# Kernel optimization log

Hardware: AMD Instinct MI355X
Metric: run time of the kernel (lower is better)

The kernel has to match this reference:

```python
import jax, jax.numpy as jnp
import numpy as np

N, D, H, L, E, P = 50000, 128, 128, 3, 640000, 100000


def setup_inputs() -> dict:
    key = jax.random.key(0)
    ks = jax.random.split(key, 10)
    x = jax.random.normal(ks[0], (N, D), dtype=jnp.float32)
    ei = jax.random.randint(ks[1], (2, E), 0, N, dtype=jnp.int64)
    pos = jax.random.randint(ks[2], (2, P), 0, N, dtype=jnp.int64)
    neg = jax.random.randint(ks[3], (2, P), 0, N, dtype=jnp.int64)
    # GCN weights: layer0 is [D,H], rest [H,H]; D==H so stack as [L,H,H]
    gcn_w = jax.random.normal(ks[4], (L, H, H), dtype=jnp.float32) / np.sqrt(H)
    gcn_b = jnp.zeros((L, H), dtype=jnp.float32)
    pred_w = jax.random.normal(ks[5], (H * L, 1), dtype=jnp.float32) / np.sqrt(H * L)
    pred_b = jnp.zeros((1,), dtype=jnp.float32)
    return {"x": x, "ei": ei, "pos": pos, "neg": neg,
            "gcn_w": gcn_w, "gcn_b": gcn_b, "pred_w": pred_w, "pred_b": pred_b}


def reference(x, ei, pos, neg, gcn_w, gcn_b, pred_w, pred_b):
    n = x.shape[0]
    loops = jnp.arange(n, dtype=ei.dtype)
    src = jnp.concatenate([ei[0], loops])  # self-loops (GCNConv default)
    dst = jnp.concatenate([ei[1], loops])
    deg = jax.ops.segment_sum(jnp.ones_like(dst, dtype=x.dtype), dst, num_segments=n)
    dinv = jax.lax.rsqrt(deg)  # deg >= 1 thanks to self-loops
    coef = (dinv[src] * dinv[dst])[:, None]  # [E+N, 1] symmetric norm

    embs = []
    h = x
    for i in range(gcn_w.shape[0]):
        hw = h @ gcn_w[i]                                   # [N, H]
        agg = jax.ops.segment_sum(hw[src] * coef, dst, num_segments=n)
        h = jax.nn.relu(agg + gcn_b[i])
        embs.append(h)
    z = jnp.concatenate(embs, axis=1)                        # [N, H*L]

    def logits(e):
        return (z[e[0]] * z[e[1]]) @ pred_w + pred_b         # [P, 1]

    pos_logit = logits(pos)
    neg_logit = logits(neg)
    # BCEWithLogitsLoss with targets [1...1, 0...0], mean reduction
    total = pos_logit.shape[0] + neg_logit.shape[0]
    loss = (jnp.sum(-jax.nn.log_sigmoid(pos_logit)) +
            jnp.sum(-jax.nn.log_sigmoid(-neg_logit))) / total
    return loss
```

## Files before the change

### kernel.cpp

```cpp
#include <hip/hip_runtime.h>
#include <hip/hip_bf16.h>

#define DD 128

typedef __attribute__((ext_vector_type(8))) short short8;
typedef __attribute__((ext_vector_type(4))) float f32x4;
typedef __attribute__((ext_vector_type(2))) float f32x2;

static __device__ __forceinline__ int gtid() {
    return blockIdx.x * blockDim.x + threadIdx.x;
}

static __device__ __forceinline__ ushort f2bfu(float f) {
    __hip_bfloat16 h = __float2bfloat16(f);
    return *reinterpret_cast<ushort*>(&h);
}

static __device__ __forceinline__ unsigned int fp8e(float f) {
    unsigned int s = (__float_as_uint(f) >> 31) << 7;
    float a = fabsf(f);
    if (a < 0.015625f) return s | (unsigned int)rintf(a * 512.0f);
    unsigned int u = __float_as_uint(a);
    u += 0x0007FFFFu + ((u >> 20) & 1u);
    unsigned int e8 = (u >> 23) - 120u;
    unsigned int m = (u >> 20) & 7u;
    if (e8 > 15u || (e8 == 15u && m == 7u)) return s | 0x7Eu;
    return s | (e8 << 3) | m;
}

static __device__ __forceinline__ float fp8d(unsigned int b) {
    unsigned int t = b & 0x7Fu;
    float v = (t >= 8u) ? __uint_as_float((t << 20) + 0x3C000000u)
                        : (float)t * 0.001953125f;
    return (b & 0x80u) ? -v : v;
}

static __device__ __forceinline__ unsigned int pk8x2(float a, float b) {
#if __has_builtin(__builtin_amdgcn_cvt_pk_fp8_f32)
    return (unsigned int)__builtin_amdgcn_cvt_pk_fp8_f32(a, b, 0, false);
#else
    return fp8e(a) | (fp8e(b) << 8);
#endif
}

static __device__ __forceinline__ unsigned int pk8x4(float a, float b, float c, float d) {
#if __has_builtin(__builtin_amdgcn_cvt_pk_fp8_f32)
    int v = __builtin_amdgcn_cvt_pk_fp8_f32(a, b, 0, false);
    v = __builtin_amdgcn_cvt_pk_fp8_f32(c, d, v, true);
    return (unsigned int)v;
#else
    return fp8e(a) | (fp8e(b) << 8) | (fp8e(c) << 16) | (fp8e(d) << 24);
#endif
}

static __device__ __forceinline__ void fp8x4_dec(unsigned int u, float* f) {
#if __has_builtin(__builtin_amdgcn_cvt_pk_f32_fp8)
    f32x2 lo = __builtin_amdgcn_cvt_pk_f32_fp8((int)u, false);
    f32x2 hi = __builtin_amdgcn_cvt_pk_f32_fp8((int)u, true);
    f[0] = lo[0]; f[1] = lo[1]; f[2] = hi[0]; f[3] = hi[1];
#else
    f[0] = fp8d(u & 0xFFu);
    f[1] = fp8d((u >> 8) & 0xFFu);
    f[2] = fp8d((u >> 16) & 0xFFu);
    f[3] = fp8d((u >> 24) & 0xFFu);
#endif
}


__global__ void count_kernel(int* __restrict__ counts, const int* __restrict__ dst, int e) {
    int i = gtid();
    if (i < e) atomicAdd(&counts[dst[i]], 1);
}

__global__ __launch_bounds__(256) void scan_blocks(const int* __restrict__ counts,
                                                   int* __restrict__ rowptr,
                                                   int* __restrict__ partial,
                                                   float* __restrict__ dinv, int n) {
    __shared__ int s[256];
    int i = blockIdx.x * 256 + threadIdx.x;
    int v = (i < n) ? counts[i] : 0;
    if (i < n) dinv[i] = rsqrtf(1.0f + (float)v);
    s[threadIdx.x] = v;
    __syncthreads();
    for (int off = 1; off < 256; off <<= 1) {
        int t = (threadIdx.x >= off) ? s[threadIdx.x - off] : 0;
        __syncthreads();
        s[threadIdx.x] += t;
        __syncthreads();
    }
    if (i < n) rowptr[i] = s[threadIdx.x] - v;
    if (threadIdx.x == 255) partial[blockIdx.x] = s[255];
}

__global__ __launch_bounds__(256) void scan_partials(int* __restrict__ partial,
                                                     int* __restrict__ partial2, int nb) {
    __shared__ int s[256];
    int v = (threadIdx.x < nb) ? partial[threadIdx.x] : 0;
    s[threadIdx.x] = v;
    __syncthreads();
    for (int off = 1; off < 256; off <<= 1) {
        int t = (threadIdx.x >= off) ? s[threadIdx.x - off] : 0;
        __syncthreads();
        s[threadIdx.x] += t;
        __syncthreads();
    }
    partial2[threadIdx.x] = s[threadIdx.x] - v;
}

__global__ __launch_bounds__(256) void add_offsets(int* __restrict__ rowptr,
                                                   int* __restrict__ cursor,
                                                   const int* __restrict__ partial2,
                                                   int n, int e) {
    int i = blockIdx.x * 256 + threadIdx.x;
    if (i < n) {
        int r = rowptr[i] + partial2[blockIdx.x];
        rowptr[i] = r;
        cursor[i] = r;
        if (i == n - 1) rowptr[n] = e;
    }
}

__global__ __launch_bounds__(256) void fill_kernel(
    const int* __restrict__ ei, int* __restrict__ cursor,
    ushort* __restrict__ csr_src, int e, int n, int blocksPerPart) {
    int part = blockIdx.x & 7;
    int blk = blockIdx.x >> 3;
    int lo = (int)(((long)n * part) >> 3);
    int hi = (int)(((long)n * (part + 1)) >> 3);
    int stride = blocksPerPart * 256;
    for (int i = blk * 256 + threadIdx.x; i < e; i += stride) {
        int d = ei[e + i];
        if (d < lo || d >= hi) continue;
        int s = ei[i];
        int pos = atomicAdd(&cursor[d], 1);
        csr_src[pos] = (ushort)s;
    }
}

__global__ void cvt_kernel(const float* __restrict__ x, unsigned char* __restrict__ xq, size_t m8) {
    size_t i = (size_t)blockIdx.x * blockDim.x + threadIdx.x;
    if (i >= m8) return;
    const float4* xp = reinterpret_cast<const float4*>(x + i * 8);
    float4 a = xp[0], b = xp[1];
    uint2 q;
    q.x = pk8x4(a.x, a.y, a.z, a.w);
    q.y = pk8x4(b.x, b.y, b.z, b.w);
    *reinterpret_cast<uint2*>(xq + i * 8) = q;
}

__global__ __launch_bounds__(256) void wpack_kernel(const float* __restrict__ gcn_w,
                                                    ushort* __restrict__ wfrag) {
    int tid = blockIdx.x * 256 + threadIdx.x;
    if (tid >= 3 * 4 * 8 * 64) return;
    int lane = tid & 63;
    int c = (tid >> 6) & 7;
    int s = (tid >> 9) & 3;
    int l = tid >> 11;
    const float* W = gcn_w + (size_t)l * 128 * 128;
    int col = c * 16 + (lane & 15);
    int k0 = s * 32 + (lane >> 4) * 8;
    ushort u[8];
#pragma unroll
    for (int j = 0; j < 8; ++j) {
        u[j] = f2bfu(W[(size_t)(k0 + j) * 128 + col]);
    }
    *reinterpret_cast<uint4*>(wfrag + (size_t)tid * 8) = *reinterpret_cast<const uint4*>(u);
}

__global__ __launch_bounds__(256) void layer_fused_kernel(
    const unsigned char* __restrict__ srcq, int srcStride,
    const int* __restrict__ rowptr, const ushort* __restrict__ csr_src,
    const float* __restrict__ dinv, const ushort* __restrict__ wfrag,
    const float* __restrict__ bias, const float* __restrict__ pwsl,
    unsigned char* __restrict__ zq_sl, unsigned char* __restrict__ zqw_sl, int n) {
    __shared__ unsigned char ah[16 * 256];
    int lane = threadIdx.x & 63;
    int wid = threadIdx.x >> 6;
    int row0 = blockIdx.x * 16;

    short8 b0[4], b1[4];
    int c0 = wid * 2;
#pragma unroll
    for (int s = 0; s < 4; ++s) {
        b0[s] = *reinterpret_cast<const short8*>(wfrag + ((size_t)(s * 8 + c0) * 64 + lane) * 8);
        b1[s] = *reinterpret_cast<const short8*>(wfrag + ((size_t)(s * 8 + c0 + 1) * 64 + lane) * 8);
    }

    int g = lane >> 3;
    int c = lane & 7;
#pragma unroll
    for (int t = 0; t < 4; ++t) {
        int lr = wid * 4 + t;
        int row = row0 + lr;
        int j0 = rowptr[row], j1 = rowptr[row + 1];
        float dr = dinv[row];
        float acc[16];
#pragma unroll
        for (int k = 0; k < 16; ++k) acc[k] = 0.f;
        for (int j = j0 + g; j < j1; j += 8) {
            int s = (int)csr_src[j];
            float cf = dinv[s] * dr;
            uint4 v = *reinterpret_cast<const uint4*>(srcq + (size_t)s * srcStride + c * 16);
            float f[16];
            fp8x4_dec(v.x, f);
            fp8x4_dec(v.y, f + 4);
            fp8x4_dec(v.z, f + 8);
            fp8x4_dec(v.w, f + 12);
#pragma unroll
            for (int k = 0; k < 16; ++k) acc[k] = fmaf(cf, f[k], acc[k]);
        }
#pragma unroll
        for (int k = 0; k < 16; ++k) {
            acc[k] += __shfl_xor(acc[k], 8);
            acc[k] += __shfl_xor(acc[k], 16);
            acc[k] += __shfl_xor(acc[k], 32);
        }
        float d2 = dr * dr;
        uint4 sv = *reinterpret_cast<const uint4*>(srcq + (size_t)row * srcStride + c * 16);
        float sf[16];
        fp8x4_dec(sv.x, sf);
        fp8x4_dec(sv.y, sf + 4);
        fp8x4_dec(sv.z, sf + 8);
        fp8x4_dec(sv.w, sf + 12);
#pragma unroll
        for (int k = 0; k < 16; ++k) acc[k] = fmaf(d2, sf[k], acc[k]);
        if (g == 0) {
            unsigned int pk[8];
#pragma unroll
            for (int q = 0; q < 8; ++q) {
                pk[q] = (unsigned int)f2bfu(acc[2 * q]) | ((unsigned int)f2bfu(acc[2 * q + 1]) << 16);
            }
            int swz = (lr & 7) << 4;
            int bo = c * 32;
            *reinterpret_cast<uint4*>(ah + lr * 256 + (bo ^ swz)) =
                *reinterpret_cast<const uint4*>(pk);
            *reinterpret_cast<uint4*>(ah + lr * 256 + ((bo + 16) ^ swz)) =
                *reinterpret_cast<const uint4*>(pk + 4);
        }
    }
    __syncthreads();

    int rlo = lane & 15;
    int kg = lane >> 4;
    int swzr = (rlo & 7) << 4;
    const unsigned char* arow = ah + rlo * 256;
    short8 a0 = *reinterpret_cast<const short8*>(arow + ((kg * 16) ^ swzr));
    short8 a1 = *reinterpret_cast<const short8*>(arow + ((kg * 16 + 64) ^ swzr));
    short8 a2 = *reinterpret_cast<const short8*>(arow + ((kg * 16 + 128) ^ swzr));
    short8 a3 = *reinterpret_cast<const short8*>(arow + ((kg * 16 + 192) ^ swzr));
    f32x4 acc0 = {0.f, 0.f, 0.f, 0.f};
    f32x4 acc1 = {0.f, 0.f, 0.f, 0.f};
    acc0 = __builtin_amdgcn_mfma_f32_16x16x32_bf16(a0, b0[0], acc0, 0, 0, 0);
    acc1 = __builtin_amdgcn_mfma_f32_16x16x32_bf16(a0, b1[0], acc1, 0, 0, 0);
    acc0 = __builtin_amdgcn_mfma_f32_16x16x32_bf16(a1, b0[1], acc0, 0, 0, 0);
    acc1 = __builtin_amdgcn_mfma_f32_16x16x32_bf16(a1, b1[1], acc1, 0, 0, 0);
    acc0 = __builtin_amdgcn_mfma_f32_16x16x32_bf16(a2, b0[2], acc0, 0, 0, 0);
    acc1 = __builtin_amdgcn_mfma_f32_16x16x32_bf16(a2, b1[2], acc1, 0, 0, 0);
    acc0 = __builtin_amdgcn_mfma_f32_16x16x32_bf16(a3, b0[3], acc0, 0, 0, 0);
    acc1 = __builtin_amdgcn_mfma_f32_16x16x32_bf16(a3, b1[3], acc1, 0, 0, 0);

    int col0 = wid * 32 + rlo;
    float bias0 = bias[col0], bias1 = bias[col0 + 16];
    float pw0 = pwsl[col0] * 8.0f, pw1 = pwsl[col0 + 16] * 8.0f;
    int rowBase = row0 + kg * 4;
#pragma unroll
    for (int r = 0; r < 4; ++r) {
        float v0 = fmaxf(acc0[r] + bias0, 0.f);
        float v1 = fmaxf(acc1[r] + bias1, 0.f);
        unsigned int q = pk8x2(v0, v1);
        unsigned char* zr = zq_sl + (size_t)(rowBase + r) * 384 + col0;
        zr[0] = (unsigned char)(q & 0xFFu);
        zr[16] = (unsigned char)((q >> 8) & 0xFFu);
        unsigned int w = pk8x2(v0 * pw0, v1 * pw1);
        unsigned char* wr = zqw_sl + (size_t)(rowBase + r) * 384 + col0;
        wr[0] = (unsigned char)(w & 0xFFu);
        wr[16] = (unsigned char)((w >> 8) & 0xFFu);
    }
}

__global__ __launch_bounds__(256) void loss_mfma_kernel(
    const unsigned char* __restrict__ zq, const unsigned char* __restrict__ zqw,
    const int* __restrict__ pos, const int* __restrict__ neg,
    const float* __restrict__ pb, float* __restrict__ partialOut,
    int p, float inv_total) {
    __shared__ float red[4];
    int lane = threadIdx.x & 63;
    int wv = threadIdx.x >> 6;
    int pairBase = (blockIdx.x * 4 + wv) * 16;
    float term = 0.f;
    if (pairBase < 2 * p) {
        int m = lane & 15;
        int kg = lane >> 4;
        int pi = pairBase + m;
        int pic = (pi < 2 * p) ? pi : (2 * p - 1);
        bool isneg = (pic >= p);
        const int* pr = isneg ? neg : pos;
        int idx = isneg ? (pic - p) : pic;
        int a = pr[idx];
        int b = pr[p + idx];
        const long* pa = reinterpret_cast<const long*>(zq + (size_t)a * 384) + kg;
        const long* pbw = reinterpret_cast<const long*>(zqw + (size_t)b * 384) + kg;
        long av[12], bv[12];
#pragma unroll
        for (int s = 0; s < 12; ++s) av[s] = pa[s * 4];
#pragma unroll
        for (int s = 0; s < 12; ++s) bv[s] = pbw[s * 4];
        f32x4 acc = {0.f, 0.f, 0.f, 0.f};
#pragma unroll
        for (int s = 0; s < 12; ++s) {
            acc = __builtin_amdgcn_mfma_f32_16x16x32_fp8_fp8(av[s], bv[s], acc, 0, 0, 0);
        }
        bool isdiag = (lane >> 4) == ((lane & 15) >> 2);
        int r2 = lane & 3;
        float v = (r2 == 0) ? acc[0] : (r2 == 1) ? acc[1] : (r2 == 2) ? acc[2] : acc[3];
        if (isdiag && pi < 2 * p) {
            float logit = v * 0.125f + pb[0];
            float t = isneg ? logit : -logit;
            term = (fmaxf(t, 0.f) + log1pf(expf(-fabsf(t)))) * inv_total;
        }
    }
#pragma unroll
    for (int off = 1; off < 64; off <<= 1) term += __shfl_xor(term, off);
    if (lane == 0) red[wv] = term;
    __syncthreads();
    if (threadIdx.x == 0) partialOut[blockIdx.x] = red[0] + red[1] + red[2] + red[3];
}

__global__ __launch_bounds__(256) void loss_reduce_kernel(
    const float* __restrict__ partial, float* __restrict__ out, int m) {
    __shared__ float s[256];
    float a = 0.f;
    for (int i = threadIdx.x; i < m; i += 256) a += partial[i];
    s[threadIdx.x] = a;
    __syncthreads();
    for (int off = 128; off > 0; off >>= 1) {
        if (threadIdx.x < off) s[threadIdx.x] += s[threadIdx.x + off];
        __syncthreads();
    }
    if (threadIdx.x == 0) out[0] = s[0];
}

extern "C" void kernel_launch(void* const* d_in, const int* in_sizes, int n_in,
                              void* d_out, int out_size, void* d_ws, size_t ws_size,
                              hipStream_t stream) {
    const float* x      = (const float*)d_in[0];
    const int*   ei     = (const int*)d_in[1];
    const int*   pos    = (const int*)d_in[2];
    const int*   neg    = (const int*)d_in[3];
    const float* gcn_w  = (const float*)d_in[4];
    const float* gcn_b  = (const float*)d_in[5];
    const float* pred_w = (const float*)d_in[6];
    const float* pred_b = (const float*)d_in[7];
    float* out = (float*)d_out;

    const int n = in_sizes[0] / DD;
    const int e = in_sizes[1] / 2;
    const int p = in_sizes[2] / 2;
    const int nb = (n + 255) / 256;

    char* ws = (char*)d_ws;
    size_t off = 0;
    auto alloc = [&](size_t bytes) {
        void* ptr = ws + off;
        off += (bytes + 255) & ~(size_t)255;
        return ptr;
    };
    float* dinv      = (float*)alloc((size_t)n * 4);
    int*   counts    = (int*)alloc((size_t)n * 4);
    int*   rowptr    = (int*)alloc((size_t)(n + 1) * 4);
    int*   cursor    = (int*)alloc((size_t)n * 4);
    int*   partial   = (int*)alloc(256 * 4);
    int*   partial2  = (int*)alloc(256 * 4);
    float* lossPart  = (float*)alloc((size_t)4096 * 4);
    ushort* csr_src  = (ushort*)alloc((size_t)e * 2);
    ushort* wfrag    = (ushort*)alloc((size_t)3 * 2048 * 8 * 2);
    unsigned char* xq = (unsigned char*)alloc((size_t)n * 128);
    unsigned char* zq  = (unsigned char*)alloc((size_t)n * 384);
    unsigned char* zqw = (unsigned char*)alloc((size_t)n * 384);
    (void)ws_size;

    hipMemsetAsync(counts, 0, (size_t)n * 4, stream);

    count_kernel<<<(e + 255) / 256, 256, 0, stream>>>(counts, ei + e, e);
    scan_blocks<<<nb, 256, 0, stream>>>(counts, rowptr, partial, dinv, n);
    scan_partials<<<1, 256, 0, stream>>>(partial, partial2, nb);
    add_offsets<<<nb, 256, 0, stream>>>(rowptr, cursor, partial2, n, e);
    int blocksPerPart = (e + 255) / 256 / 2;
    fill_kernel<<<blocksPerPart * 8, 256, 0, stream>>>(ei, cursor, csr_src, e, n, blocksPerPart);

    size_t m8 = (size_t)n * 128 / 8;
    cvt_kernel<<<(int)((m8 + 255) / 256), 256, 0, stream>>>(x, xq, m8);
    wpack_kernel<<<24, 256, 0, stream>>>(gcn_w, wfrag);

    const int layerBlocks = n / 16;
    for (int l = 0; l < 3; ++l) {
        const unsigned char* srcq = (l == 0) ? xq : (zq + (size_t)(l - 1) * 128);
        int srcStride = (l == 0) ? 128 : 384;
        layer_fused_kernel<<<layerBlocks, 256, 0, stream>>>(
            srcq, srcStride, rowptr, csr_src, dinv,
            wfrag + (size_t)l * 2048 * 8,
            gcn_b + (size_t)l * 128, pred_w + (size_t)l * 128,
            zq + (size_t)l * 128, zqw + (size_t)l * 128, n);
    }

    float inv_total = 1.0f / (2.0f * (float)p);
    int lossBlocks = (2 * p + 63) / 64;
    loss_mfma_kernel<<<lossBlocks, 256, 0, stream>>>(
        zq, zqw, pos, neg, pred_b, lossPart, p, inv_total);
    loss_reduce_kernel<<<1, 256, 0, stream>>>(lossPart, out, lossBlocks);
}
```

Measured before the change: 264.0 us.

## Use 1024-thread blocks with one wave per row in fused GCN layer

The fused layer kernel moves from 256 threads (4 waves, each aggregating 4 rows serially) to 1024 threads (16 waves, each aggregating one row). After the barrier, 8 waves each compute one 16-column MFMA tile and the other 8 exit. This exposes more parallel gather work per block and shortens each wave's serial loop. In exchange, blocks are larger, which may reduce occupancy flexibility, half the waves sit idle during the MFMA phase, and the output stores become single-byte writes per lane.

```diff
diff --git a/kernel.cpp b/kernel.cpp
--- a/kernel.cpp
+++ b/kernel.cpp
@@ -167,7 +167,7 @@
     *reinterpret_cast<uint4*>(wfrag + (size_t)tid * 8) = *reinterpret_cast<const uint4*>(u);
 }
 
-__global__ __launch_bounds__(256) void layer_fused_kernel(
+__global__ __launch_bounds__(1024) void layer_fused_kernel(
     const unsigned char* __restrict__ srcq, int srcStride,
     const int* __restrict__ rowptr, const ushort* __restrict__ csr_src,
     const float* __restrict__ dinv, const ushort* __restrict__ wfrag,
@@ -178,20 +178,10 @@
     int wid = threadIdx.x >> 6;
     int row0 = blockIdx.x * 16;
 
-    short8 b0[4], b1[4];
-    int c0 = wid * 2;
-#pragma unroll
-    for (int s = 0; s < 4; ++s) {
-        b0[s] = *reinterpret_cast<const short8*>(wfrag + ((size_t)(s * 8 + c0) * 64 + lane) * 8);
-        b1[s] = *reinterpret_cast<const short8*>(wfrag + ((size_t)(s * 8 + c0 + 1) * 64 + lane) * 8);
-    }
-
-    int g = lane >> 3;
-    int c = lane & 7;
-#pragma unroll
-    for (int t = 0; t < 4; ++t) {
-        int lr = wid * 4 + t;
-        int row = row0 + lr;
+    {
+        int g = lane >> 3;
+        int c = lane & 7;
+        int row = row0 + wid;
         int j0 = rowptr[row], j1 = rowptr[row + 1];
         float dr = dinv[row];
         float acc[16];
@@ -230,16 +220,22 @@
             for (int q = 0; q < 8; ++q) {
                 pk[q] = (unsigned int)f2bfu(acc[2 * q]) | ((unsigned int)f2bfu(acc[2 * q + 1]) << 16);
             }
-            int swz = (lr & 7) << 4;
+            int swz = (wid & 7) << 4;
             int bo = c * 32;
-            *reinterpret_cast<uint4*>(ah + lr * 256 + (bo ^ swz)) =
+            *reinterpret_cast<uint4*>(ah + wid * 256 + (bo ^ swz)) =
                 *reinterpret_cast<const uint4*>(pk);
-            *reinterpret_cast<uint4*>(ah + lr * 256 + ((bo + 16) ^ swz)) =
+            *reinterpret_cast<uint4*>(ah + wid * 256 + ((bo + 16) ^ swz)) =
                 *reinterpret_cast<const uint4*>(pk + 4);
         }
     }
     __syncthreads();
-
+    if (wid >= 8) return;
+
+    short8 bfr[4];
+#pragma unroll
+    for (int s = 0; s < 4; ++s) {
+        bfr[s] = *reinterpret_cast<const short8*>(wfrag + ((size_t)(s * 8 + wid) * 64 + lane) * 8);
+    }
     int rlo = lane & 15;
     int kg = lane >> 4;
     int swzr = (rlo & 7) << 4;
@@ -248,33 +244,22 @@
     short8 a1 = *reinterpret_cast<const short8*>(arow + ((kg * 16 + 64) ^ swzr));
     short8 a2 = *reinterpret_cast<const short8*>(arow + ((kg * 16 + 128) ^ swzr));
     short8 a3 = *reinterpret_cast<const short8*>(arow + ((kg * 16 + 192) ^ swzr));
-    f32x4 acc0 = {0.f, 0.f, 0.f, 0.f};
-    f32x4 acc1 = {0.f, 0.f, 0.f, 0.f};
-    acc0 = __builtin_amdgcn_mfma_f32_16x16x32_bf16(a0, b0[0], acc0, 0, 0, 0);
-    acc1 = __builtin_amdgcn_mfma_f32_16x16x32_bf16(a0, b1[0], acc1, 0, 0, 0);
-    acc0 = __builtin_amdgcn_mfma_f32_16x16x32_bf16(a1, b0[1], acc0, 0, 0, 0);
-    acc1 = __builtin_amdgcn_mfma_f32_16x16x32_bf16(a1, b1[1], acc1, 0, 0, 0);
-    acc0 = __builtin_amdgcn_mfma_f32_16x16x32_bf16(a2, b0[2], acc0, 0, 0, 0);
-    acc1 = __builtin_amdgcn_mfma_f32_16x16x32_bf16(a2, b1[2], acc1, 0, 0, 0);
-    acc0 = __builtin_amdgcn_mfma_f32_16x16x32_bf16(a3, b0[3], acc0, 0, 0, 0);
-    acc1 = __builtin_amdgcn_mfma_f32_16x16x32_bf16(a3, b1[3], acc1, 0, 0, 0);
-
-    int col0 = wid * 32 + rlo;
-    float bias0 = bias[col0], bias1 = bias[col0 + 16];
-    float pw0 = pwsl[col0] * 8.0f, pw1 = pwsl[col0 + 16] * 8.0f;
+    f32x4 acc = {0.f, 0.f, 0.f, 0.f};
+    acc = __builtin_amdgcn_mfma_f32_16x16x32_bf16(a0, bfr[0], acc, 0, 0, 0);
+    acc = __builtin_amdgcn_mfma_f32_16x16x32_bf16(a1, bfr[1], acc, 0, 0, 0);
+    acc = __builtin_amdgcn_mfma_f32_16x16x32_bf16(a2, bfr[2], acc, 0, 0, 0);
+    acc = __builtin_amdgcn_mfma_f32_16x16x32_bf16(a3, bfr[3], acc, 0, 0, 0);
+
+    int col = wid * 16 + rlo;
+    float b0 = bias[col];
+    float pw = pwsl[col] * 8.0f;
     int rowBase = row0 + kg * 4;
 #pragma unroll
     for (int r = 0; r < 4; ++r) {
-        float v0 = fmaxf(acc0[r] + bias0, 0.f);
-        float v1 = fmaxf(acc1[r] + bias1, 0.f);
-        unsigned int q = pk8x2(v0, v1);
-        unsigned char* zr = zq_sl + (size_t)(rowBase + r) * 384 + col0;
-        zr[0] = (unsigned char)(q & 0xFFu);
-        zr[16] = (unsigned char)((q >> 8) & 0xFFu);
-        unsigned int w = pk8x2(v0 * pw0, v1 * pw1);
-        unsigned char* wr = zqw_sl + (size_t)(rowBase + r) * 384 + col0;
-        wr[0] = (unsigned char)(w & 0xFFu);
-        wr[16] = (unsigned char)((w >> 8) & 0xFFu);
+        float v = fmaxf(acc[r] + b0, 0.f);
+        unsigned int q = pk8x2(v, v * pw);
+        zq_sl[(size_t)(rowBase + r) * 384 + col] = (unsigned char)(q & 0xFFu);
+        zqw_sl[(size_t)(rowBase + r) * 384 + col] = (unsigned char)((q >> 8) & 0xFFu);
     }
 }
 
@@ -396,7 +381,7 @@
     for (int l = 0; l < 3; ++l) {
         const unsigned char* srcq = (l == 0) ? xq : (zq + (size_t)(l - 1) * 128);
         int srcStride = (l == 0) ? 128 : 384;
-        layer_fused_kernel<<<layerBlocks, 256, 0, stream>>>(
+        layer_fused_kernel<<<layerBlocks, 1024, 0, stream>>>(
             srcq, srcStride, rowptr, csr_src, dinv,
             wfrag + (size_t)l * 2048 * 8,
             gcn_b + (size_t)l * 128, pred_w + (size_t)l * 128,
```

Measured after the change: 237.3 us. 1.11x faster.
